# Performance work log

Hardware: AMD Instinct MI355X
Metric: run time of the kernel (lower is better)

The kernel has to match this reference:

```python
import jax, jax.numpy as jnp
import numpy as np

B, R, N, M, K = 4, 4, 4096, 64, 3
F_NUM = 512
KN = K * N


def _block(x, Ws, bs):
    """SO-Net PointResNet: 1x1 convs + ReLU; last layer sees concat(input, hidden)."""
    h = x
    for W, b in zip(Ws[:-1], bs[:-1]):
        h = jax.nn.relu(jnp.einsum('oc,bcn->bon', W, h) + b[None, :, None])
    h = jnp.concatenate([x, h], axis=1)
    return jax.nn.relu(jnp.einsum('oc,bcn->bon', Ws[-1], h) + bs[-1][None, :, None])


def _forward(x, intensity, node, node_knn_I, fpW, fpB, gpW, gpB):
    # --- som.query_topk: k nearest SOM nodes per point ---
    xd = jax.lax.stop_gradient(x)
    dist = jnp.sum((xd[:, :, :, None] - node[:, :, None, :]) ** 2, axis=1)      # B,N,M
    _, topk = jax.lax.top_k(-dist, K)                                           # B,N,K
    min_idx = topk.transpose(0, 2, 1).reshape(B, KN)                            # B,KN (k copies stacked)
    mask = jax.nn.one_hot(min_idx, M, dtype=jnp.float32)                        # B,KN,M
    mask_row_max = jnp.max(mask, axis=1) > 0                                    # B,M  node has >=1 point
    mask_row_sum = jnp.sum(mask, axis=1)                                        # B,M  points per node

    x_stack = jnp.tile(x, (1, 1, K))                                            # B,2,KN
    cluster_mean = jnp.einsum('bcn,bnm->bcm', jax.lax.stop_gradient(x_stack), mask) \
                   / (mask_row_sum[:, None, :] + 1e-5)                          # B,2,M (detached)

    # --- rotation group (2x2 rotations at angles 2*pi*r/R) ---
    theta = 2.0 * jnp.pi * jnp.arange(R, dtype=jnp.float32) / R
    c, s = jnp.cos(theta), jnp.sin(theta)
    rot = jnp.stack([jnp.stack([c, -s], -1), jnp.stack([s, c], -1)], -2)        # R,2,2

    x_rot = jnp.einsum('rij,bjn->brin', rot, x_stack)                           # B,R,2,KN
    node_rot = jnp.einsum('rij,bjm->brim', rot, cluster_mean)                   # B,R,2,M
    centers = jnp.take_along_axis(node_rot, min_idx[:, None, None, :], axis=3)  # B,R,2,KN
    x_dec = jax.lax.stop_gradient(x_rot - centers).reshape(B * R, 2, KN)

    # --- first PointResNet over all B*R rotation copies ---
    feat = _block(x_dec, fpW, fpB)                                              # BR,128,KN

    # --- index_max scatter-max per SOM cluster (value of argmax == segment max) ---
    seg = jnp.tile(min_idx[:, None, :], (1, R, 1)).reshape(B * R, KN)
    segmax = jax.vmap(lambda f, sgi: jax.ops.segment_max(f.T, sgi, num_segments=M).T)(feat, seg)
    rowmax = jnp.tile(mask_row_max[:, None, :], (1, R, 1)).reshape(B * R, M)
    pooled = jnp.where(rowmax[:, None, :], segmax, feat[:, :, 0:1])             # BR,128,M (empty -> gather idx 0)

    # --- final PointResNet over SOM nodes, then max over nodes and rotations ---
    g_in = jnp.concatenate([node_rot.reshape(B * R, 2, M), pooled], axis=1)     # BR,130,M
    out = _block(g_in, gpW, gpB)                                                # BR,F,M
    return out.reshape(B, R, F_NUM, M).max(axis=3).max(axis=1)                  # B,F


def setup_inputs() -> dict:
    key = jax.random.key(0)
    ks = jax.random.split(key, 24)
    d = {}
    d['x'] = jax.random.normal(ks[0], (B, 2, N), jnp.float32)
    d['intensity'] = jax.random.uniform(ks[1], (B, 1, N), jnp.float32)
    d['node'] = jax.random.normal(ks[2], (B, 2, M), jnp.float32)
    d['node_knn_I'] = jax.random.randint(ks[3], (B, M, 1), 0, M)
    dims_fp = [(64, 2), (64, 64), (128, 64), (128, 130)]      # PointResNet(2,[64,64,128,128])
    dims_gp = [(256, 130), (256, 256), (512, 256), (F_NUM, 642)]  # PointResNet(130,[256,256,512,F])
    i = 4
    for name, dims in (('fp', dims_fp), ('gp', dims_gp)):
        for j, (o, ci) in enumerate(dims):
            d[f'{name}_W{j}'] = jax.random.normal(ks[i], (o, ci), jnp.float32) / np.sqrt(ci).astype(np.float32)
            d[f'{name}_b{j}'] = jnp.zeros((o,), jnp.float32)
            i += 1
    return d


def reference(x, intensity, node, node_knn_I,
              fp_W0, fp_b0, fp_W1, fp_b1, fp_W2, fp_b2, fp_W3, fp_b3,
              gp_W0, gp_b0, gp_W1, gp_b1, gp_W2, gp_b2, gp_W3, gp_b3):
    return _forward(x, intensity, node, node_knn_I,
                    [fp_W0, fp_W1, fp_W2, fp_W3], [fp_b0, fp_b1, fp_b2, fp_b3],
                    [gp_W0, gp_W1, gp_W2, gp_W3], [gp_b0, gp_b1, gp_b2, gp_b3])
```

## Files before the change

kernel.cpp:

```cpp
#include <hip/hip_runtime.h>
#include <stdint.h>

#define BB 4
#define RR 4
#define NN 4096
#define MM 64
#define KK 3
#define KNN 12288
#define BRR 16
#define FF 512

typedef short bf16x8 __attribute__((ext_vector_type(8)));
typedef float f32x4 __attribute__((ext_vector_type(4)));

__device__ __forceinline__ float bf2f(unsigned int u) {
  union { unsigned int i; float f; } v; v.i = u << 16; return v.f;
}
__device__ __forceinline__ unsigned short f2bf(float f) {
  union { float f; unsigned int i; } v; v.f = f;
  unsigned int x = v.i;
  return (unsigned short)((x + 0x7fffu + ((x >> 16) & 1u)) >> 16);
}
__device__ __forceinline__ unsigned int cvtpk(float a, float b) {
  unsigned int r;
  asm("v_cvt_pk_bf16_f32 %0, %1, %2" : "=v"(r) : "v"(a), "v"(b));
  return r;
}
__device__ __forceinline__ float ldf(const void* p, long i, int isbf) {
  if (isbf) return bf2f(((const unsigned short*)p)[i]);
  return ((const float*)p)[i];
}
__device__ __forceinline__ int hsw(int col, int so) { return col * 72  + (so ^ (col & 24)); }
__device__ __forceinline__ int csw(int col, int so) { return col * 136 + (so ^ (col & 24)); }

struct WPtrs { const void* p[7]; };

__global__ __launch_bounds__(256) void k_front(
    const void* __restrict__ x, const void* __restrict__ node, WPtrs wp,
    int* __restrict__ flag, unsigned short* __restrict__ Wb,
    int* __restrict__ idx, float* __restrict__ csum, int* __restrict__ blkcnt) {
  __shared__ int bad;
  __shared__ float nd[2][64];
  __shared__ float cs[192];
  int tid = threadIdx.x;
  if (tid == 0) bad = 0;
  __syncthreads();
  {
    const unsigned short* xs = (const unsigned short*)x;
    int cnt = 0;
    for (int i = tid; i < 1024; i += 256) {
      unsigned short u = xs[i * 2];
      int e = (u >> 7) & 0xFF;
      if (e >= 0x90 || (e > 0 && e <= 0x50)) ++cnt;
    }
    atomicAdd(&bad, cnt);
  }
  __syncthreads();
  int isbf = (bad < 100) ? 1 : 0;
  if (blockIdx.x == 0 && tid == 0) flag[0] = isbf;

  if (blockIdx.x < 2295) {
    const int e0=4096, e1=12288, e2=28928, e3=62208, e4=127744, e5=258816, e6=587520;
    int t = blockIdx.x * 256 + tid;
    if (t >= e6) return;
    int s, base;
    if      (t < e0) { s=0; base=0;  }
    else if (t < e1) { s=1; base=e0; }
    else if (t < e2) { s=2; base=e1; }
    else if (t < e3) { s=3; base=e2; }
    else if (t < e4) { s=4; base=e3; }
    else if (t < e5) { s=5; base=e4; }
    else             { s=6; base=e5; }
    int local = t - base;
    unsigned short u;
    if (isbf) u = ((const unsigned short*)wp.p[s])[local];
    else      u = f2bf(((const float*)wp.p[s])[local]);
    Wb[t] = u;
    return;
  }
  int bi = blockIdx.x - 2295;
  int b = bi >> 4;
  int n = ((bi & 15) << 8) + tid;
  if (tid < 128) nd[tid >> 6][tid & 63] = ldf(node, b * 128 + tid, isbf);
  if (tid < 192) cs[tid] = 0.f;
  __syncthreads();
  float x0 = ldf(x, b * 8192 + n, isbf);
  float x1 = ldf(x, b * 8192 + 4096 + n, isbf);
  float d0 = 1e30f, d1 = 1e30f, d2 = 1e30f;
  int m0 = 0, m1 = 0, m2 = 0;
#pragma unroll 8
  for (int m = 0; m < 64; ++m) {
    float dx = x0 - nd[0][m];
    float dy = x1 - nd[1][m];
    float d = __fmul_rn(dx, dx) + __fmul_rn(dy, dy);
    if (d < d0)      { d2=d1; m2=m1; d1=d0; m1=m0; d0=d; m0=m; }
    else if (d < d1) { d2=d1; m2=m1; d1=d;  m1=m; }
    else if (d < d2) { d2=d;  m2=m; }
  }
  long base = ((long)b * NN + n) * 3;
  idx[base] = m0; idx[base + 1] = m1; idx[base + 2] = m2;
  atomicAdd(&cs[m0*3+0], x0); atomicAdd(&cs[m0*3+1], x1); atomicAdd(&cs[m0*3+2], 1.f);
  atomicAdd(&cs[m1*3+0], x0); atomicAdd(&cs[m1*3+1], x1); atomicAdd(&cs[m1*3+2], 1.f);
  atomicAdd(&cs[m2*3+0], x0); atomicAdd(&cs[m2*3+1], x1); atomicAdd(&cs[m2*3+2], 1.f);
  __syncthreads();
  if (tid < 192) atomicAdd(&csum[b * 192 + tid], cs[tid]);
  if (tid < 64) blkcnt[bi * 64 + tid] = (int)cs[tid*3 + 2];
}

__global__ __launch_bounds__(256) void k_scatter2(
    const float* __restrict__ csum, const int* __restrict__ blkcnt,
    const int* __restrict__ idx, int* __restrict__ sorted,
    float* __restrict__ noderot, int* __restrict__ rowflag) {
  __shared__ int scnt[64];
  __shared__ int soff[64];
  __shared__ int lc[64];
  int tid = threadIdx.x;
  int blk = blockIdx.x;
  int b = blk >> 4, chunk = blk & 15;
  if (tid < 64) scnt[tid] = (int)csum[b*192 + tid*3 + 2];
  __syncthreads();
  if (tid < 64) {
    int m = tid, acc = 0;
    for (int mm = 0; mm < m; ++mm) acc += scnt[mm];
    for (int c = 0; c < chunk; ++c) acc += blkcnt[(b*16 + c)*64 + m];
    soff[m] = acc;
    lc[m] = 0;
    if (chunk == 0) {
      float s0 = csum[b*192 + m*3], s1 = csum[b*192 + m*3 + 1], cc = csum[b*192 + m*3 + 2];
      float mx = s0 / (cc + 1e-5f);
      float my = s1 / (cc + 1e-5f);
      rowflag[b*64 + m] = (cc > 0.f) ? 1 : 0;
      for (int r = 0; r < 4; ++r) {
        float th = 1.5707964f * (float)r;
        float cr = cosf(th), sr = sinf(th);
        noderot[((b*4 + r)*2 + 0)*64 + m] = cr*mx - sr*my;
        noderot[((b*4 + r)*2 + 1)*64 + m] = sr*mx + cr*my;
      }
    }
  }
  __syncthreads();
  int n = ((blk & 15) << 8) + tid;
#pragma unroll
  for (int kk = 0; kk < 3; ++kk) {
    int m = idx[((long)b * NN + n) * 3 + kk];
    int pos = atomicAdd(&lc[m], 1);
    sorted[b * KNN + soff[m] + pos] = (m << 12) | n;
  }
}

__global__ __launch_bounds__(256) void k_fused(
    const void* __restrict__ x, const int* __restrict__ sorted,
    const int* __restrict__ idx, const float* __restrict__ noderot,
    const int* __restrict__ flag,
    const void* __restrict__ fW0, const void* __restrict__ fb0,
    const unsigned short* __restrict__ Wb,
    const void* __restrict__ fb1, const void* __restrict__ fb2,
    const void* __restrict__ fb3,
    unsigned int* __restrict__ pooled, float* __restrict__ feat0) {
  __shared__ unsigned short Cs[64 * 136];
  __shared__ unsigned short Hs[64 * 72];
  __shared__ int mcol[64];
  const unsigned short* fW1 = Wb;
  const unsigned short* fW2 = Wb + 4096;
  const unsigned short* fW3 = Wb + 12288;
  int isbf = flag[0];
  int tid = threadIdx.x, lane = tid & 63, wv = tid >> 6;
  int quad = lane >> 4, lr = lane & 15;
  int br = blockIdx.y, b = br >> 2, r = br & 3;
  if (tid < 64) {
    int e = sorted[b * KNN + blockIdx.x * 64 + tid];
    int m = e >> 12, n = e & 4095;
    int isz = (n == 0 && m == idx[(long)b * NN * 3]) ? 256 : 0;
    mcol[tid] = m | isz;
    float x0 = ldf(x, b*8192 + n, isbf), x1 = ldf(x, b*8192 + 4096 + n, isbf);
    float th = 1.5707964f * (float)r;
    float cr = cosf(th), sr = sinf(th);
    float xd0 = (cr*x0 - sr*x1) - noderot[(br*2 + 0)*64 + m];
    float xd1 = (sr*x0 + cr*x1) - noderot[(br*2 + 1)*64 + m];
    *(unsigned int*)&Cs[csw(tid, 0)] = cvtpk(xd0, xd1);
  }
  __syncthreads();
  {
    int col = tid & 63, og = (tid >> 6) << 4;
    unsigned int xu = *(unsigned int*)&Cs[csw(col, 0)];
    float fx0 = bf2f(xu & 0xffff), fx1 = bf2f(xu >> 16);
    float hv[16];
#pragma unroll
    for (int j = 0; j < 16; ++j) {
      int o = og + j;
      float h = ldf(fb0, o, isbf) + ldf(fW0, o*2, isbf) * fx0 + ldf(fW0, o*2+1, isbf) * fx1;
      hv[j] = fmaxf(h, 0.f);
    }
    union { bf16x8 v; unsigned int u[4]; } o8[2];
#pragma unroll
    for (int j = 0; j < 16; j += 2) o8[j >> 3].u[(j & 7) >> 1] = cvtpk(hv[j], hv[j+1]);
    *(bf16x8*)&Hs[hsw(col, og)]     = o8[0].v;
    *(bf16x8*)&Hs[hsw(col, og + 8)] = o8[1].v;
  }
  __syncthreads();
  {
    int o0 = wv * 16;
    f32x4 acc[4];
    float bb4[4];
#pragma unroll
    for (int rr = 0; rr < 4; ++rr) bb4[rr] = ldf(fb1, o0 + quad*4 + rr, isbf);
#pragma unroll
    for (int nt = 0; nt < 4; ++nt) acc[nt] = (f32x4){bb4[0], bb4[1], bb4[2], bb4[3]};
#pragma unroll
    for (int ks = 0; ks < 64; ks += 32) {
      bf16x8 a = *(const bf16x8*)(fW1 + (o0 + lr)*64 + ks + quad*8);
#pragma unroll
      for (int nt = 0; nt < 4; ++nt) {
        bf16x8 bf = *(bf16x8*)&Hs[hsw(nt*16 + lr, ks + quad*8)];
        acc[nt] = __builtin_amdgcn_mfma_f32_16x16x32_bf16(a, bf, acc[nt], 0, 0, 0);
      }
    }
    __syncthreads();
#pragma unroll
    for (int nt = 0; nt < 4; ++nt) {
      int col = nt*16 + lr;
      unsigned int lo = cvtpk(fmaxf(acc[nt][0], 0.f), fmaxf(acc[nt][1], 0.f));
      unsigned int hi = cvtpk(fmaxf(acc[nt][2], 0.f), fmaxf(acc[nt][3], 0.f));
      *(unsigned long long*)&Hs[hsw(col, o0 + quad*4)] =
          (unsigned long long)lo | ((unsigned long long)hi << 32);
    }
  }
  __syncthreads();
#pragma unroll
  for (int p2 = 0; p2 < 2; ++p2) {
    int o0 = p2*64 + wv*16;
    f32x4 acc[4];
    float bb4[4];
#pragma unroll
    for (int rr = 0; rr < 4; ++rr) bb4[rr] = ldf(fb2, o0 + quad*4 + rr, isbf);
#pragma unroll
    for (int nt = 0; nt < 4; ++nt) acc[nt] = (f32x4){bb4[0], bb4[1], bb4[2], bb4[3]};
#pragma unroll
    for (int ks = 0; ks < 64; ks += 32) {
      bf16x8 a = *(const bf16x8*)(fW2 + (o0 + lr)*64 + ks + quad*8);
#pragma unroll
      for (int nt = 0; nt < 4; ++nt) {
        bf16x8 bf = *(bf16x8*)&Hs[hsw(nt*16 + lr, ks + quad*8)];
        acc[nt] = __builtin_amdgcn_mfma_f32_16x16x32_bf16(a, bf, acc[nt], 0, 0, 0);
      }
    }
#pragma unroll
    for (int nt = 0; nt < 4; ++nt) {
      int col = nt*16 + lr;
      int o = o0 + quad*4;
      unsigned int w0 = cvtpk(fmaxf(acc[nt][0], 0.f), fmaxf(acc[nt][1], 0.f));
      unsigned int w1 = cvtpk(fmaxf(acc[nt][2], 0.f), fmaxf(acc[nt][3], 0.f));
      int so0 = 2 + o;
      int so1 = 4 + o;
      *(unsigned int*)&Cs[csw(col, so0)] = w0;
      *(unsigned int*)&Cs[(so1 < 128) ? csw(col, so1) : (col*136 + so1)] = w1;
    }
  }
  __syncthreads();
  f32x4 acc3[2][4];
#pragma unroll
  for (int p3 = 0; p3 < 2; ++p3) {
    int o0 = p3*64 + wv*16;
    float bb4[4];
#pragma unroll
    for (int rr = 0; rr < 4; ++rr) bb4[rr] = ldf(fb3, o0 + quad*4 + rr, isbf);
#pragma unroll
    for (int nt = 0; nt < 4; ++nt) acc3[p3][nt] = (f32x4){bb4[0], bb4[1], bb4[2], bb4[3]};
#pragma unroll
    for (int ks = 0; ks < 128; ks += 32) {
      union { bf16x8 v; unsigned int u[4]; } au;
      const unsigned int* ap = (const unsigned int*)(fW3 + (long)(o0 + lr)*130 + ks + quad*8);
      au.u[0] = ap[0]; au.u[1] = ap[1]; au.u[2] = ap[2]; au.u[3] = ap[3];
#pragma unroll
      for (int nt = 0; nt < 4; ++nt) {
        bf16x8 bf = *(bf16x8*)&Cs[csw(nt*16 + lr, ks + quad*8)];
        acc3[p3][nt] = __builtin_amdgcn_mfma_f32_16x16x32_bf16(au.v, bf, acc3[p3][nt], 0, 0, 0);
      }
    }
#pragma unroll
    for (int rr = 0; rr < 4; ++rr) {
      int o = o0 + quad*4 + rr;
      unsigned int wu = *(const unsigned int*)(fW3 + (long)o*130 + 128);
      float w0 = bf2f(wu & 0xffff), w1 = bf2f(wu >> 16);
#pragma unroll
      for (int nt = 0; nt < 4; ++nt) {
        unsigned int bu = *(unsigned int*)&Cs[(nt*16 + lr)*136 + 128];
        acc3[p3][nt][rr] += w0 * bf2f(bu & 0xffff) + w1 * bf2f(bu >> 16);
      }
    }
  }
  __syncthreads();
#pragma unroll
  for (int p3 = 0; p3 < 2; ++p3) {
    int o0 = p3*64 + wv*16;
#pragma unroll
    for (int nt = 0; nt < 4; ++nt) {
      int col = nt*16 + lr;
      unsigned int lo = cvtpk(fmaxf(acc3[p3][nt][0], 0.f), fmaxf(acc3[p3][nt][1], 0.f));
      unsigned int hi = cvtpk(fmaxf(acc3[p3][nt][2], 0.f), fmaxf(acc3[p3][nt][3], 0.f));
      *(unsigned long long*)&Cs[csw(col, o0 + quad*4)] =
          (unsigned long long)lo | ((unsigned long long)hi << 32);
    }
  }
  __syncthreads();
  {
    int o = tid & 127, h = tid >> 7;
    int c0 = h * 32;
    int curm = mcol[c0] & 255;
    float v = 0.f;
    for (int c = c0; c < c0 + 32; ++c) {
      int mc = mcol[c];
      int mm = mc & 255;
      float f = bf2f(Cs[csw(c, o)]);
      if (mm != curm) {
        atomicMax(&pooled[(((long)br*64 + curm) << 7) + o], __float_as_uint(v));
        curm = mm; v = 0.f;
      }
      v = fmaxf(v, f);
      if (mc & 256) feat0[br*128 + o] = f;
    }
    atomicMax(&pooled[(((long)br*64 + curm) << 7) + o], __float_as_uint(v));
  }
}

template<int OT, int KW, int KMAIN, bool REM2, int DSTR, int DOFF, int EPI>
__device__ __forceinline__ void gp_layer(
    const unsigned short* __restrict__ W, const void* __restrict__ bias, int isbf,
    const unsigned short* Bs, int bstr, unsigned short* Ds,
    int wv, int quad, int lr, int b, unsigned int* __restrict__ outmax) {
#pragma unroll
  for (int ot = 0; ot < OT; ++ot) {
    int o0 = (wv * OT + ot) * 16;
    float bb4[4];
#pragma unroll
    for (int rr = 0; rr < 4; ++rr) bb4[rr] = ldf(bias, o0 + quad*4 + rr, isbf);
    f32x4 acc = (f32x4){bb4[0], bb4[1], bb4[2], bb4[3]};
    const unsigned short* arow = W + (long)(o0 + lr) * KW;
    for (int ks = 0; ks < KMAIN; ks += 32) {
      bf16x8 a;
      if constexpr ((KW % 8) == 0) {
        a = *(const bf16x8*)(arow + ks + quad*8);
      } else {
        union { bf16x8 v; unsigned int u[4]; } au;
        const unsigned int* ap = (const unsigned int*)(arow + ks + quad*8);
        au.u[0] = ap[0]; au.u[1] = ap[1]; au.u[2] = ap[2]; au.u[3] = ap[3];
        a = au.v;
      }
      bf16x8 bf = *(const bf16x8*)(Bs + lr * bstr + ks + quad*8);
      acc = __builtin_amdgcn_mfma_f32_16x16x32_bf16(a, bf, acc, 0, 0, 0);
    }
    if constexpr (REM2) {
      unsigned int bu = *(const unsigned int*)(Bs + lr * bstr + KMAIN);
      float b0 = bf2f(bu & 0xffff), b1 = bf2f(bu >> 16);
#pragma unroll
      for (int rr = 0; rr < 4; ++rr) {
        int o = o0 + quad*4 + rr;
        unsigned int wu = *(const unsigned int*)(W + (long)o * KW + KMAIN);
        acc[rr] += bf2f(wu & 0xffff) * b0 + bf2f(wu >> 16) * b1;
      }
    }
    if constexpr (EPI == 0) {
      unsigned int lo = cvtpk(fmaxf(acc[0], 0.f), fmaxf(acc[1], 0.f));
      unsigned int hi = cvtpk(fmaxf(acc[2], 0.f), fmaxf(acc[3], 0.f));
      unsigned short* op = Ds + lr * DSTR + DOFF + o0 + quad*4;
      if constexpr ((DOFF & 3) == 0) {
        *(unsigned long long*)op = (unsigned long long)lo | ((unsigned long long)hi << 32);
      } else {
        *(unsigned int*)op       = lo;
        *(unsigned int*)(op + 2) = hi;
      }
    } else {
#pragma unroll
      for (int rr = 0; rr < 4; ++rr) {
        float v = fmaxf(acc[rr], 0.f);
        v = fmaxf(v, __shfl_xor(v, 1, 64));
        v = fmaxf(v, __shfl_xor(v, 2, 64));
        v = fmaxf(v, __shfl_xor(v, 4, 64));
        v = fmaxf(v, __shfl_xor(v, 8, 64));
        if (lr == 0)
          atomicMax(&outmax[b * FF + o0 + quad*4 + rr], __float_as_uint(v));
      }
    }
  }
}

__global__ __launch_bounds__(512) void k_gp(
    const unsigned int* __restrict__ pooled, const float* __restrict__ feat0,
    const int* __restrict__ rowflag, const float* __restrict__ noderot,
    const int* __restrict__ flag, const unsigned short* __restrict__ Wb,
    const void* __restrict__ gpb0, const void* __restrict__ gpb1,
    const void* __restrict__ gpb2, const void* __restrict__ gpb3,
    unsigned int* __restrict__ outmax) {
  __shared__ unsigned short G3[16 * 648];
  __shared__ unsigned short H1[16 * 264];
  __shared__ unsigned short H2[16 * 264];
  const unsigned short* gW0 = Wb + 28928;
  const unsigned short* gW1 = Wb + 62208;
  const unsigned short* gW2 = Wb + 127744;
  const unsigned short* gW3 = Wb + 258816;
  int isbf = flag[0];
  int tid = threadIdx.x, lane = tid & 63, wv = tid >> 6;
  int quad = lane >> 4, lr = lane & 15;
  int c0 = blockIdx.x * 16;
  int br = c0 >> 6, b = br >> 2;
  {
    int j = tid >> 5, oq = (tid & 31) << 2;
    int col = c0 + j, m = col & 63;
    int fl = rowflag[b * 64 + m];
    float v[4];
#pragma unroll
    for (int i = 0; i < 4; ++i) {
      float pv = __uint_as_float(pooled[((long)col << 7) + oq + i]);
      v[i] = fl ? pv : feat0[br * 128 + oq + i];
    }
    *(unsigned int*)&G3[j * 648 + 2 + oq] = cvtpk(v[0], v[1]);
    *(unsigned int*)&G3[j * 648 + 4 + oq] = cvtpk(v[2], v[3]);
    if (tid < 32) {
      int jj = tid >> 1, o = tid & 1;
      int mm = (c0 + jj) & 63;
      G3[jj * 648 + o] = f2bf(noderot[(br * 2 + o) * 64 + mm]);
    }
  }
  __syncthreads();
  gp_layer<2, 130, 128, true,  264, 0,   0>(gW0, gpb0, isbf, G3, 648, H1, wv, quad, lr, b, outmax);
  __syncthreads();
  gp_layer<2, 256, 256, false, 264, 0,   0>(gW1, gpb1, isbf, H1, 264, H2, wv, quad, lr, b, outmax);
  __syncthreads();
  gp_layer<4, 256, 256, false, 648, 130, 0>(gW2, gpb2, isbf, H2, 264, G3, wv, quad, lr, b, outmax);
  __syncthreads();
  gp_layer<4, 642, 640, true,  0,   0,   1>(gW3, gpb3, isbf, G3, 648, nullptr, wv, quad, lr, b, outmax);
}

__global__ __launch_bounds__(256) void k_out(
    const unsigned int* __restrict__ outmax, const int* __restrict__ flag,
    void* __restrict__ out) {
  int t = blockIdx.x * 256 + threadIdx.x;
  float v = __uint_as_float(outmax[t]);
  if (flag[0]) ((unsigned short*)out)[t] = f2bf(v);
  else         ((float*)out)[t] = v;
}

extern "C" void kernel_launch(void* const* d_in, const int* in_sizes, int n_in,
                              void* d_out, int out_size, void* d_ws, size_t ws_size,
                              hipStream_t stream) {
  const void* x    = d_in[0];
  const void* node = d_in[2];
  const void* fpW0 = d_in[4];  const void* fpb0 = d_in[5];
  const void* fpW1 = d_in[6];  const void* fpb1 = d_in[7];
  const void* fpW2 = d_in[8];  const void* fpb2 = d_in[9];
  const void* fpW3 = d_in[10]; const void* fpb3 = d_in[11];
  const void* gpW0 = d_in[12]; const void* gpb0 = d_in[13];
  const void* gpW1 = d_in[14]; const void* gpb1 = d_in[15];
  const void* gpW2 = d_in[16]; const void* gpb2 = d_in[17];
  const void* gpW3 = d_in[18]; const void* gpb3 = d_in[19];

  char* ws = (char*)d_ws;
  int*            flag    = (int*)(ws + 0);
  float*          csum    = (float*)(ws + 256);
  unsigned int*   outmax  = (unsigned int*)(ws + 3328);
  unsigned int*   pooled  = (unsigned int*)(ws + 11520);
  int*            idx     = (int*)(ws + 535808);
  int*            blkcnt  = (int*)(ws + 732416);
  float*          noderot = (float*)(ws + 766208);
  int*            rowflag = (int*)(ws + 774400);
  int*            sorted  = (int*)(ws + 775424);
  float*          feat0   = (float*)(ws + 972032);
  unsigned short* Wb      = (unsigned short*)(ws + 3355904);

  hipMemsetAsync(ws, 0, 535808, stream);

  WPtrs wp; wp.p[0]=fpW1; wp.p[1]=fpW2; wp.p[2]=fpW3; wp.p[3]=gpW0;
  wp.p[4]=gpW1; wp.p[5]=gpW2; wp.p[6]=gpW3;
  k_front<<<2359, 256, 0, stream>>>(x, node, wp, flag, Wb, idx, csum, blkcnt);
  k_scatter2<<<64, 256, 0, stream>>>(csum, blkcnt, idx, sorted, noderot, rowflag);
  k_fused<<<dim3(192, 16), 256, 0, stream>>>(x, sorted, idx, noderot, flag,
                                             fpW0, fpb0, Wb, fpb1, fpb2, fpb3,
                                             pooled, feat0);
  k_gp<<<64, 512, 0, stream>>>(pooled, feat0, rowflag, noderot, flag, Wb,
                               gpb0, gpb1, gpb2, gpb3, outmax);
  k_out<<<8, 256, 0, stream>>>(outmax, flag, d_out);
}
```

Measured before the change: 203.1 us.

## Persist fused pointnet blocks over four tiles with register-resident weights; restructure gp_layer loop

k_fused now launches a quarter of the blocks. Each block loops over four 64-point tiles and loads the W1/W2/W3 MFMA operand fragments into registers once, before the loop, instead of reloading them per tile. gp_layer is reorganised so the B operand is loaded once per k-step and shared across all OT output tiles, with the A loads batched ahead of the MFMAs. The trade-offs are higher register pressure (around 28 bf16x8 weight fragments per thread), fewer concurrent blocks in k_fused, and an extra barrier per tile.

After: 263.7 us. 29.9% more time.

```diff
diff --git a/kernel.cpp b/kernel.cpp
--- a/kernel.cpp
+++ b/kernel.cpp
@@ -167,159 +167,182 @@
   int tid = threadIdx.x, lane = tid & 63, wv = tid >> 6;
   int quad = lane >> 4, lr = lane & 15;
   int br = blockIdx.y, b = br >> 2, r = br & 3;
-  if (tid < 64) {
-    int e = sorted[b * KNN + blockIdx.x * 64 + tid];
-    int m = e >> 12, n = e & 4095;
-    int isz = (n == 0 && m == idx[(long)b * NN * 3]) ? 256 : 0;
-    mcol[tid] = m | isz;
-    float x0 = ldf(x, b*8192 + n, isbf), x1 = ldf(x, b*8192 + 4096 + n, isbf);
-    float th = 1.5707964f * (float)r;
-    float cr = cosf(th), sr = sinf(th);
-    float xd0 = (cr*x0 - sr*x1) - noderot[(br*2 + 0)*64 + m];
-    float xd1 = (sr*x0 + cr*x1) - noderot[(br*2 + 1)*64 + m];
-    *(unsigned int*)&Cs[csw(tid, 0)] = cvtpk(xd0, xd1);
-  }
-  __syncthreads();
-  {
-    int col = tid & 63, og = (tid >> 6) << 4;
-    unsigned int xu = *(unsigned int*)&Cs[csw(col, 0)];
-    float fx0 = bf2f(xu & 0xffff), fx1 = bf2f(xu >> 16);
-    float hv[16];
-#pragma unroll
-    for (int j = 0; j < 16; ++j) {
-      int o = og + j;
-      float h = ldf(fb0, o, isbf) + ldf(fW0, o*2, isbf) * fx0 + ldf(fW0, o*2+1, isbf) * fx1;
-      hv[j] = fmaxf(h, 0.f);
-    }
-    union { bf16x8 v; unsigned int u[4]; } o8[2];
-#pragma unroll
-    for (int j = 0; j < 16; j += 2) o8[j >> 3].u[(j & 7) >> 1] = cvtpk(hv[j], hv[j+1]);
-    *(bf16x8*)&Hs[hsw(col, og)]     = o8[0].v;
-    *(bf16x8*)&Hs[hsw(col, og + 8)] = o8[1].v;
-  }
-  __syncthreads();
-  {
-    int o0 = wv * 16;
-    f32x4 acc[4];
-    float bb4[4];
-#pragma unroll
-    for (int rr = 0; rr < 4; ++rr) bb4[rr] = ldf(fb1, o0 + quad*4 + rr, isbf);
-#pragma unroll
-    for (int nt = 0; nt < 4; ++nt) acc[nt] = (f32x4){bb4[0], bb4[1], bb4[2], bb4[3]};
-#pragma unroll
-    for (int ks = 0; ks < 64; ks += 32) {
-      bf16x8 a = *(const bf16x8*)(fW1 + (o0 + lr)*64 + ks + quad*8);
+  int o1 = wv * 16;
+  bf16x8 aW1[2], aW2[2][2], aW3[2][4];
+  unsigned int tw3[2][4];
+#pragma unroll
+  for (int ks2 = 0; ks2 < 2; ++ks2)
+    aW1[ks2] = *(const bf16x8*)(fW1 + (o1 + lr)*64 + ks2*32 + quad*8);
+#pragma unroll
+  for (int p2 = 0; p2 < 2; ++p2)
+#pragma unroll
+    for (int ks2 = 0; ks2 < 2; ++ks2)
+      aW2[p2][ks2] = *(const bf16x8*)(fW2 + (p2*64 + o1 + lr)*64 + ks2*32 + quad*8);
+#pragma unroll
+  for (int p3 = 0; p3 < 2; ++p3) {
+#pragma unroll
+    for (int ks4 = 0; ks4 < 4; ++ks4) {
+      union { bf16x8 v; unsigned int u[4]; } au;
+      const unsigned int* ap =
+          (const unsigned int*)(fW3 + (long)(p3*64 + o1 + lr)*130 + ks4*32 + quad*8);
+      au.u[0] = ap[0]; au.u[1] = ap[1]; au.u[2] = ap[2]; au.u[3] = ap[3];
+      aW3[p3][ks4] = au.v;
+    }
+#pragma unroll
+    for (int rr = 0; rr < 4; ++rr)
+      tw3[p3][rr] = *(const unsigned int*)(fW3 + (long)(p3*64 + o1 + quad*4 + rr)*130 + 128);
+  }
+
+#pragma unroll 1
+  for (int t = 0; t < 4; ++t) {
+    int xb = (blockIdx.x << 2) + t;
+    if (tid < 64) {
+      int e = sorted[b * KNN + xb * 64 + tid];
+      int m = e >> 12, n = e & 4095;
+      int isz = (n == 0 && m == idx[(long)b * NN * 3]) ? 256 : 0;
+      mcol[tid] = m | isz;
+      float x0 = ldf(x, b*8192 + n, isbf), x1 = ldf(x, b*8192 + 4096 + n, isbf);
+      float th = 1.5707964f * (float)r;
+      float cr = cosf(th), sr = sinf(th);
+      float xd0 = (cr*x0 - sr*x1) - noderot[(br*2 + 0)*64 + m];
+      float xd1 = (sr*x0 + cr*x1) - noderot[(br*2 + 1)*64 + m];
+      *(unsigned int*)&Cs[csw(tid, 0)] = cvtpk(xd0, xd1);
+    }
+    __syncthreads();
+    {
+      int col = tid & 63, og = (tid >> 6) << 4;
+      unsigned int xu = *(unsigned int*)&Cs[csw(col, 0)];
+      float fx0 = bf2f(xu & 0xffff), fx1 = bf2f(xu >> 16);
+      float hv[16];
+#pragma unroll
+      for (int j = 0; j < 16; ++j) {
+        int o = og + j;
+        float h = ldf(fb0, o, isbf) + ldf(fW0, o*2, isbf) * fx0 + ldf(fW0, o*2+1, isbf) * fx1;
+        hv[j] = fmaxf(h, 0.f);
+      }
+      union { bf16x8 v; unsigned int u[4]; } o8[2];
+#pragma unroll
+      for (int j = 0; j < 16; j += 2) o8[j >> 3].u[(j & 7) >> 1] = cvtpk(hv[j], hv[j+1]);
+      *(bf16x8*)&Hs[hsw(col, og)]     = o8[0].v;
+      *(bf16x8*)&Hs[hsw(col, og + 8)] = o8[1].v;
+    }
+    __syncthreads();
+    {
+      f32x4 acc[4];
+      float bb4[4];
+#pragma unroll
+      for (int rr = 0; rr < 4; ++rr) bb4[rr] = ldf(fb1, o1 + quad*4 + rr, isbf);
+#pragma unroll
+      for (int nt = 0; nt < 4; ++nt) acc[nt] = (f32x4){bb4[0], bb4[1], bb4[2], bb4[3]};
+#pragma unroll
+      for (int ks2 = 0; ks2 < 2; ++ks2) {
+#pragma unroll
+        for (int nt = 0; nt < 4; ++nt) {
+          bf16x8 bf = *(bf16x8*)&Hs[hsw(nt*16 + lr, ks2*32 + quad*8)];
+          acc[nt] = __builtin_amdgcn_mfma_f32_16x16x32_bf16(aW1[ks2], bf, acc[nt], 0, 0, 0);
+        }
+      }
+      __syncthreads();
 #pragma unroll
       for (int nt = 0; nt < 4; ++nt) {
-        bf16x8 bf = *(bf16x8*)&Hs[hsw(nt*16 + lr, ks + quad*8)];
-        acc[nt] = __builtin_amdgcn_mfma_f32_16x16x32_bf16(a, bf, acc[nt], 0, 0, 0);
-      }
-    }
-    __syncthreads();
-#pragma unroll
-    for (int nt = 0; nt < 4; ++nt) {
-      int col = nt*16 + lr;
-      unsigned int lo = cvtpk(fmaxf(acc[nt][0], 0.f), fmaxf(acc[nt][1], 0.f));
-      unsigned int hi = cvtpk(fmaxf(acc[nt][2], 0.f), fmaxf(acc[nt][3], 0.f));
-      *(unsigned long long*)&Hs[hsw(col, o0 + quad*4)] =
-          (unsigned long long)lo | ((unsigned long long)hi << 32);
-    }
-  }
-  __syncthreads();
-#pragma unroll
-  for (int p2 = 0; p2 < 2; ++p2) {
-    int o0 = p2*64 + wv*16;
-    f32x4 acc[4];
-    float bb4[4];
-#pragma unroll
-    for (int rr = 0; rr < 4; ++rr) bb4[rr] = ldf(fb2, o0 + quad*4 + rr, isbf);
-#pragma unroll
-    for (int nt = 0; nt < 4; ++nt) acc[nt] = (f32x4){bb4[0], bb4[1], bb4[2], bb4[3]};
-#pragma unroll
-    for (int ks = 0; ks < 64; ks += 32) {
-      bf16x8 a = *(const bf16x8*)(fW2 + (o0 + lr)*64 + ks + quad*8);
+        int col = nt*16 + lr;
+        unsigned int lo = cvtpk(fmaxf(acc[nt][0], 0.f), fmaxf(acc[nt][1], 0.f));
+        unsigned int hi = cvtpk(fmaxf(acc[nt][2], 0.f), fmaxf(acc[nt][3], 0.f));
+        *(unsigned long long*)&Hs[hsw(col, o1 + quad*4)] =
+            (unsigned long long)lo | ((unsigned long long)hi << 32);
+      }
+    }
+    __syncthreads();
+#pragma unroll
+    for (int p2 = 0; p2 < 2; ++p2) {
+      int o0 = p2*64 + o1;
+      f32x4 acc[4];
+      float bb4[4];
+#pragma unroll
+      for (int rr = 0; rr < 4; ++rr) bb4[rr] = ldf(fb2, o0 + quad*4 + rr, isbf);
+#pragma unroll
+      for (int nt = 0; nt < 4; ++nt) acc[nt] = (f32x4){bb4[0], bb4[1], bb4[2], bb4[3]};
+#pragma unroll
+      for (int ks2 = 0; ks2 < 2; ++ks2) {
+#pragma unroll
+        for (int nt = 0; nt < 4; ++nt) {
+          bf16x8 bf = *(bf16x8*)&Hs[hsw(nt*16 + lr, ks2*32 + quad*8)];
+          acc[nt] = __builtin_amdgcn_mfma_f32_16x16x32_bf16(aW2[p2][ks2], bf, acc[nt], 0, 0, 0);
+        }
+      }
 #pragma unroll
       for (int nt = 0; nt < 4; ++nt) {
-        bf16x8 bf = *(bf16x8*)&Hs[hsw(nt*16 + lr, ks + quad*8)];
-        acc[nt] = __builtin_amdgcn_mfma_f32_16x16x32_bf16(a, bf, acc[nt], 0, 0, 0);
-      }
-    }
-#pragma unroll
-    for (int nt = 0; nt < 4; ++nt) {
-      int col = nt*16 + lr;
-      int o = o0 + quad*4;
-      unsigned int w0 = cvtpk(fmaxf(acc[nt][0], 0.f), fmaxf(acc[nt][1], 0.f));
-      unsigned int w1 = cvtpk(fmaxf(acc[nt][2], 0.f), fmaxf(acc[nt][3], 0.f));
-      int so0 = 2 + o;
-      int so1 = 4 + o;
-      *(unsigned int*)&Cs[csw(col, so0)] = w0;
-      *(unsigned int*)&Cs[(so1 < 128) ? csw(col, so1) : (col*136 + so1)] = w1;
-    }
-  }
-  __syncthreads();
-  f32x4 acc3[2][4];
-#pragma unroll
-  for (int p3 = 0; p3 < 2; ++p3) {
-    int o0 = p3*64 + wv*16;
-    float bb4[4];
-#pragma unroll
-    for (int rr = 0; rr < 4; ++rr) bb4[rr] = ldf(fb3, o0 + quad*4 + rr, isbf);
-#pragma unroll
-    for (int nt = 0; nt < 4; ++nt) acc3[p3][nt] = (f32x4){bb4[0], bb4[1], bb4[2], bb4[3]};
-#pragma unroll
-    for (int ks = 0; ks < 128; ks += 32) {
-      union { bf16x8 v; unsigned int u[4]; } au;
-      const unsigned int* ap = (const unsigned int*)(fW3 + (long)(o0 + lr)*130 + ks + quad*8);
-      au.u[0] = ap[0]; au.u[1] = ap[1]; au.u[2] = ap[2]; au.u[3] = ap[3];
+        int col = nt*16 + lr;
+        int o = o0 + quad*4;
+        unsigned int w0 = cvtpk(fmaxf(acc[nt][0], 0.f), fmaxf(acc[nt][1], 0.f));
+        unsigned int w1 = cvtpk(fmaxf(acc[nt][2], 0.f), fmaxf(acc[nt][3], 0.f));
+        int so0 = 2 + o;
+        int so1 = 4 + o;
+        *(unsigned int*)&Cs[csw(col, so0)] = w0;
+        *(unsigned int*)&Cs[(so1 < 128) ? csw(col, so1) : (col*136 + so1)] = w1;
+      }
+    }
+    __syncthreads();
+    f32x4 acc3[2][4];
+#pragma unroll
+    for (int p3 = 0; p3 < 2; ++p3) {
+      int o0 = p3*64 + o1;
+      float bb4[4];
+#pragma unroll
+      for (int rr = 0; rr < 4; ++rr) bb4[rr] = ldf(fb3, o0 + quad*4 + rr, isbf);
+#pragma unroll
+      for (int nt = 0; nt < 4; ++nt) acc3[p3][nt] = (f32x4){bb4[0], bb4[1], bb4[2], bb4[3]};
+#pragma unroll
+      for (int ks4 = 0; ks4 < 4; ++ks4) {
+#pragma unroll
+        for (int nt = 0; nt < 4; ++nt) {
+          bf16x8 bf = *(bf16x8*)&Cs[csw(nt*16 + lr, ks4*32 + quad*8)];
+          acc3[p3][nt] = __builtin_amdgcn_mfma_f32_16x16x32_bf16(aW3[p3][ks4], bf, acc3[p3][nt], 0, 0, 0);
+        }
+      }
+#pragma unroll
+      for (int rr = 0; rr < 4; ++rr) {
+        float w0 = bf2f(tw3[p3][rr] & 0xffff), w1 = bf2f(tw3[p3][rr] >> 16);
+#pragma unroll
+        for (int nt = 0; nt < 4; ++nt) {
+          unsigned int bu = *(unsigned int*)&Cs[(nt*16 + lr)*136 + 128];
+          acc3[p3][nt][rr] += w0 * bf2f(bu & 0xffff) + w1 * bf2f(bu >> 16);
+        }
+      }
+    }
+    __syncthreads();
+#pragma unroll
+    for (int p3 = 0; p3 < 2; ++p3) {
+      int o0 = p3*64 + o1;
 #pragma unroll
       for (int nt = 0; nt < 4; ++nt) {
-        bf16x8 bf = *(bf16x8*)&Cs[csw(nt*16 + lr, ks + quad*8)];
-        acc3[p3][nt] = __builtin_amdgcn_mfma_f32_16x16x32_bf16(au.v, bf, acc3[p3][nt], 0, 0, 0);
-      }
-    }
-#pragma unroll
-    for (int rr = 0; rr < 4; ++rr) {
-      int o = o0 + quad*4 + rr;
-      unsigned int wu = *(const unsigned int*)(fW3 + (long)o*130 + 128);
-      float w0 = bf2f(wu & 0xffff), w1 = bf2f(wu >> 16);
-#pragma unroll
-      for (int nt = 0; nt < 4; ++nt) {
-        unsigned int bu = *(unsigned int*)&Cs[(nt*16 + lr)*136 + 128];
-        acc3[p3][nt][rr] += w0 * bf2f(bu & 0xffff) + w1 * bf2f(bu >> 16);
-      }
-    }
-  }
-  __syncthreads();
-#pragma unroll
-  for (int p3 = 0; p3 < 2; ++p3) {
-    int o0 = p3*64 + wv*16;
-#pragma unroll
-    for (int nt = 0; nt < 4; ++nt) {
-      int col = nt*16 + lr;
-      unsigned int lo = cvtpk(fmaxf(acc3[p3][nt][0], 0.f), fmaxf(acc3[p3][nt][1], 0.f));
-      unsigned int hi = cvtpk(fmaxf(acc3[p3][nt][2], 0.f), fmaxf(acc3[p3][nt][3], 0.f));
-      *(unsigned long long*)&Cs[csw(col, o0 + quad*4)] =
-          (unsigned long long)lo | ((unsigned long long)hi << 32);
-    }
-  }
-  __syncthreads();
-  {
-    int o = tid & 127, h = tid >> 7;
-    int c0 = h * 32;
-    int curm = mcol[c0] & 255;
-    float v = 0.f;
-    for (int c = c0; c < c0 + 32; ++c) {
-      int mc = mcol[c];
-      int mm = mc & 255;
-      float f = bf2f(Cs[csw(c, o)]);
-      if (mm != curm) {
-        atomicMax(&pooled[(((long)br*64 + curm) << 7) + o], __float_as_uint(v));
-        curm = mm; v = 0.f;
-      }
-      v = fmaxf(v, f);
-      if (mc & 256) feat0[br*128 + o] = f;
-    }
-    atomicMax(&pooled[(((long)br*64 + curm) << 7) + o], __float_as_uint(v));
+        int col = nt*16 + lr;
+        unsigned int lo = cvtpk(fmaxf(acc3[p3][nt][0], 0.f), fmaxf(acc3[p3][nt][1], 0.f));
+        unsigned int hi = cvtpk(fmaxf(acc3[p3][nt][2], 0.f), fmaxf(acc3[p3][nt][3], 0.f));
+        *(unsigned long long*)&Cs[csw(col, o0 + quad*4)] =
+            (unsigned long long)lo | ((unsigned long long)hi << 32);
+      }
+    }
+    __syncthreads();
+    {
+      int o = tid & 127, h = tid >> 7;
+      int c0 = h * 32;
+      int curm = mcol[c0] & 255;
+      float v = 0.f;
+      for (int c = c0; c < c0 + 32; ++c) {
+        int mc = mcol[c];
+        int mm = mc & 255;
+        float f = bf2f(Cs[csw(c, o)]);
+        if (mm != curm) {
+          atomicMax(&pooled[(((long)br*64 + curm) << 7) + o], __float_as_uint(v));
+          curm = mm; v = 0.f;
+        }
+        v = fmaxf(v, f);
+        if (mc & 256) feat0[br*128 + o] = f;
+      }
+      atomicMax(&pooled[(((long)br*64 + curm) << 7) + o], __float_as_uint(v));
+    }
+    __syncthreads();
   }
 }
 
@@ -328,40 +351,54 @@
     const unsigned short* __restrict__ W, const void* __restrict__ bias, int isbf,
     const unsigned short* Bs, int bstr, unsigned short* Ds,
     int wv, int quad, int lr, int b, unsigned int* __restrict__ outmax) {
+  f32x4 acc[OT];
 #pragma unroll
   for (int ot = 0; ot < OT; ++ot) {
     int o0 = (wv * OT + ot) * 16;
     float bb4[4];
 #pragma unroll
     for (int rr = 0; rr < 4; ++rr) bb4[rr] = ldf(bias, o0 + quad*4 + rr, isbf);
-    f32x4 acc = (f32x4){bb4[0], bb4[1], bb4[2], bb4[3]};
-    const unsigned short* arow = W + (long)(o0 + lr) * KW;
-    for (int ks = 0; ks < KMAIN; ks += 32) {
-      bf16x8 a;
+    acc[ot] = (f32x4){bb4[0], bb4[1], bb4[2], bb4[3]};
+  }
+  const unsigned short* brow = Bs + lr * bstr;
+  for (int ks = 0; ks < KMAIN; ks += 32) {
+    bf16x8 bf = *(const bf16x8*)(brow + ks + quad*8);
+    bf16x8 a[OT];
+#pragma unroll
+    for (int ot = 0; ot < OT; ++ot) {
+      const unsigned short* arow = W + (long)((wv * OT + ot) * 16 + lr) * KW;
       if constexpr ((KW % 8) == 0) {
-        a = *(const bf16x8*)(arow + ks + quad*8);
+        a[ot] = *(const bf16x8*)(arow + ks + quad*8);
       } else {
         union { bf16x8 v; unsigned int u[4]; } au;
         const unsigned int* ap = (const unsigned int*)(arow + ks + quad*8);
         au.u[0] = ap[0]; au.u[1] = ap[1]; au.u[2] = ap[2]; au.u[3] = ap[3];
-        a = au.v;
-      }
-      bf16x8 bf = *(const bf16x8*)(Bs + lr * bstr + ks + quad*8);
-      acc = __builtin_amdgcn_mfma_f32_16x16x32_bf16(a, bf, acc, 0, 0, 0);
-    }
-    if constexpr (REM2) {
-      unsigned int bu = *(const unsigned int*)(Bs + lr * bstr + KMAIN);
-      float b0 = bf2f(bu & 0xffff), b1 = bf2f(bu >> 16);
+        a[ot] = au.v;
+      }
+    }
+#pragma unroll
+    for (int ot = 0; ot < OT; ++ot)
+      acc[ot] = __builtin_amdgcn_mfma_f32_16x16x32_bf16(a[ot], bf, acc[ot], 0, 0, 0);
+  }
+  if constexpr (REM2) {
+    unsigned int bu = *(const unsigned int*)(brow + KMAIN);
+    float b0 = bf2f(bu & 0xffff), b1 = bf2f(bu >> 16);
+#pragma unroll
+    for (int ot = 0; ot < OT; ++ot) {
 #pragma unroll
       for (int rr = 0; rr < 4; ++rr) {
-        int o = o0 + quad*4 + rr;
+        int o = (wv * OT + ot) * 16 + quad*4 + rr;
         unsigned int wu = *(const unsigned int*)(W + (long)o * KW + KMAIN);
-        acc[rr] += bf2f(wu & 0xffff) * b0 + bf2f(wu >> 16) * b1;
-      }
-    }
+        acc[ot][rr] += bf2f(wu & 0xffff) * b0 + bf2f(wu >> 16) * b1;
+      }
+    }
+  }
+#pragma unroll
+  for (int ot = 0; ot < OT; ++ot) {
+    int o0 = (wv * OT + ot) * 16;
     if constexpr (EPI == 0) {
-      unsigned int lo = cvtpk(fmaxf(acc[0], 0.f), fmaxf(acc[1], 0.f));
-      unsigned int hi = cvtpk(fmaxf(acc[2], 0.f), fmaxf(acc[3], 0.f));
+      unsigned int lo = cvtpk(fmaxf(acc[ot][0], 0.f), fmaxf(acc[ot][1], 0.f));
+      unsigned int hi = cvtpk(fmaxf(acc[ot][2], 0.f), fmaxf(acc[ot][3], 0.f));
       unsigned short* op = Ds + lr * DSTR + DOFF + o0 + quad*4;
       if constexpr ((DOFF & 3) == 0) {
         *(unsigned long long*)op = (unsigned long long)lo | ((unsigned long long)hi << 32);
@@ -372,7 +409,7 @@
     } else {
 #pragma unroll
       for (int rr = 0; rr < 4; ++rr) {
-        float v = fmaxf(acc[rr], 0.f);
+        float v = fmaxf(acc[ot][rr], 0.f);
         v = fmaxf(v, __shfl_xor(v, 1, 64));
         v = fmaxf(v, __shfl_xor(v, 2, 64));
         v = fmaxf(v, __shfl_xor(v, 4, 64));
@@ -473,9 +510,9 @@
   wp.p[4]=gpW1; wp.p[5]=gpW2; wp.p[6]=gpW3;
   k_front<<<2359, 256, 0, stream>>>(x, node, wp, flag, Wb, idx, csum, blkcnt);
   k_scatter2<<<64, 256, 0, stream>>>(csum, blkcnt, idx, sorted, noderot, rowflag);
-  k_fused<<<dim3(192, 16), 256, 0, stream>>>(x, sorted, idx, noderot, flag,
-                                             fpW0, fpb0, Wb, fpb1, fpb2, fpb3,
-                                             pooled, feat0);
+  k_fused<<<dim3(48, 16), 256, 0, stream>>>(x, sorted, idx, noderot, flag,
+                                            fpW0, fpb0, Wb, fpb1, fpb2, fpb3,
+                                            pooled, feat0);
   k_gp<<<64, 512, 0, stream>>>(pooled, feat0, rowflag, noderot, flag, Wb,
                                gpb0, gpb1, gpb2, gpb3, outmax);
   k_out<<<8, 256, 0, stream>>>(outmax, flag, d_out);
```
